# Optimization experiments

Measured on AMD Instinct MI355X. Metric: run time of the kernel, lower is better.

## Reference

```python
import jax, jax.numpy as jnp
import numpy as np
from math import sqrt

LOCAL_WINDOW = 32
STRIDE = 64


def _sparse_mask(L):
    # L_Q == L_K path of DozerAttention:
    #  - local window: diagonals at offsets 0..local_window//2 (both signs)
    #  - strided: diagonals at offsets 0, stride+1, 2*(stride+1), ... (both signs)
    i = jnp.arange(L)[:, None]
    j = jnp.arange(L)[None, :]
    d = jnp.abs(i - j)
    local = d <= (LOCAL_WINDOW // 2)
    strided = (d % (STRIDE + 1)) == 0
    return (local | strided).astype(jnp.float32)  # [L, L]


def setup_inputs() -> dict:
    key = jax.random.key(0)
    B, L, H, D = 2, 2048, 8, 64
    kq, kk, kv = jax.random.split(key, 3)
    queries = jax.random.normal(kq, (B, L, H, D), dtype=jnp.float32)
    keys = jax.random.normal(kk, (B, L, H, D), dtype=jnp.float32)
    values = jax.random.normal(kv, (B, L, H, D), dtype=jnp.float32)
    # TriangularCausalMask: True above the diagonal -> masked with -inf
    causal = jnp.triu(jnp.ones((L, L), dtype=bool), k=1)
    attn_mask = jnp.broadcast_to(causal[None, None], (B, 1, L, L))
    return {"queries": queries, "keys": keys, "values": values, "attn_mask": attn_mask}


def reference(queries, keys, values, attn_mask):
    B, L, H, D = queries.shape
    scale = 1.0 / sqrt(D)
    sm = _sparse_mask(L)  # [L, L]
    # Original fills a zero-initialized dense score tensor only at selected key
    # columns per query row; equivalent to dense QK^T elementwise-masked by sm
    # (non-selected entries stay exactly 0, NOT -inf -- faithful quirk).
    scores = jnp.einsum('blhe,bshe->bhls', queries, keys) * sm  # [B,H,L,L]
    scores = jnp.where(attn_mask, -jnp.inf, scores)
    A = jax.nn.softmax(scale * scores, axis=-1)  # dropout p=0.0 in this config
    V = jnp.einsum('bhls,bshd->blhd', A, values)  # [B,L,H,D]
    return V
```

## Files before the change

### kernel.cpp

```cpp
#include <hip/hip_runtime.h>
#include <hip/hip_bf16.h>

#define B_ 2
#define L_ 2048
#define H_ 8
#define D_ 64
#define SP_ 65
#define NC_ 128
#define NL2_ 8
#define RS_ 512

typedef __attribute__((ext_vector_type(8))) short bf16x8;
typedef __attribute__((ext_vector_type(16))) float f32x16;

static __device__ inline short f2bf(float x) {
    return __builtin_bit_cast(short, __float2bfloat16(x));
}

static __device__ inline bf16x8 ld8_bf16(const float* __restrict__ p) {
    float4 a = *(const float4*)p;
    float4 b = *(const float4*)(p + 4);
    bf16x8 r;
    r[0]=f2bf(a.x); r[1]=f2bf(a.y); r[2]=f2bf(a.z); r[3]=f2bf(a.w);
    r[4]=f2bf(b.x); r[5]=f2bf(b.y); r[6]=f2bf(b.z); r[7]=f2bf(b.w);
    return r;
}

static __device__ inline bf16x8 ones_frag() {
    bf16x8 r;
    short o = f2bf(1.f);
    #pragma unroll
    for (int t = 0; t < 8; ++t) r[t] = o;
    return r;
}

__global__ __launch_bounds__(256) void pre_strided_k(const float* __restrict__ q,
                                                     const float* __restrict__ kk,
                                                     const float* __restrict__ v,
                                                     float* __restrict__ csum1,
                                                     float* __restrict__ csum2,
                                                     float* __restrict__ pB,
                                                     float* __restrict__ zB) {
    __shared__ float Pw[4][32][36];
    int wib  = threadIdx.x >> 6;
    int lane = threadIdx.x & 63;
    int blk  = blockIdx.x;

    if (blk < 260) {
        int u  = blk * 4 + wib;
        int bh = u / SP_;
        int r  = u % SP_;
        int h = bh & 7, b = bh >> 3;
        int half = lane >> 5, ln = lane & 31;
        const size_t base = (size_t)b * L_ * RS_ + (size_t)h * D_;

        bf16x8 bv0[2], bv1[2];
        #pragma unroll
        for (int kb = 0; kb < 2; ++kb) {
            int k0 = kb * 16 + half * 8;
            #pragma unroll
            for (int jj = 0; jj < 8; ++jj) {
                int lv = r + SP_ * (k0 + jj);
                lv = lv > L_ - 1 ? L_ - 1 : lv;
                const float* vr = v + base + (size_t)lv * RS_;
                bv0[kb][jj] = f2bf(vr[ln]);
                bv1[kb][jj] = f2bf(vr[32 + ln]);
            }
        }

        int lq = r + SP_ * ln;
        int lqc = lq > L_ - 1 ? L_ - 1 : lq;
        const float* qrow = q  + base + (size_t)lqc * RS_;
        const float* krow = kk + base + (size_t)lqc * RS_;
        f32x16 acc = {};
        #pragma unroll
        for (int kb = 0; kb < 4; ++kb) {
            bf16x8 a  = ld8_bf16(qrow + kb * 16 + half * 8);
            bf16x8 bb = ld8_bf16(krow + kb * 16 + half * 8);
            acc = __builtin_amdgcn_mfma_f32_32x32x16_bf16(a, bb, acc, 0, 0, 0);
        }
        #pragma unroll
        for (int rg = 0; rg < 16; ++rg) {
            int m = (rg & 3) + 8 * (rg >> 2) + 4 * half;
            bool act = (ln < m) && (r + SP_ * m < L_);
            Pw[wib][m][ln] = act ? (__expf(0.125f * acc[rg]) - 1.f) : 0.f;
        }
        __syncthreads();

        f32x16 p0 = {}; f32x16 p1 = {}; f32x16 po = {};
        bf16x8 ones = ones_frag();
        #pragma unroll
        for (int kb = 0; kb < 2; ++kb) {
            int k0 = kb * 16 + half * 8;
            const float* pr = &Pw[wib][ln][k0];
            float4 x = *(const float4*)pr;
            float4 y = *(const float4*)(pr + 4);
            bf16x8 ap;
            ap[0]=f2bf(x.x); ap[1]=f2bf(x.y); ap[2]=f2bf(x.z); ap[3]=f2bf(x.w);
            ap[4]=f2bf(y.x); ap[5]=f2bf(y.y); ap[6]=f2bf(y.z); ap[7]=f2bf(y.w);
            p0 = __builtin_amdgcn_mfma_f32_32x32x16_bf16(ap, bv0[kb], p0, 0, 0, 0);
            p1 = __builtin_amdgcn_mfma_f32_32x32x16_bf16(ap, bv1[kb], p1, 0, 0, 0);
            po = __builtin_amdgcn_mfma_f32_32x32x16_bf16(ap, ones,    po, 0, 0, 0);
        }
        float* pBr = pB + (size_t)bh * L_ * D_;
        float* zBr = zB + (size_t)bh * L_;
        #pragma unroll
        for (int rg = 0; rg < 16; ++rg) {
            int m = (rg & 3) + 8 * (rg >> 2) + 4 * half;
            int l = r + SP_ * m;
            if (l < L_) {
                pBr[(size_t)l * D_ + ln]      = p0[rg];
                pBr[(size_t)l * D_ + 32 + ln] = p1[rg];
                if (ln == 0) zBr[l] = po[rg];
            }
        }
    } else if (blk < 772) {
        int u = (blk - 260) * 4 + wib;
        int c = u & (NC_ - 1);
        int bh = u >> 7;
        int h = bh & 7, b = bh >> 3;
        const float* vb = v + (size_t)(b * L_ + c * 16) * RS_ + h * D_ + lane;
        float s = 0.f;
        #pragma unroll
        for (int l = 0; l < 16; ++l) s += vb[l * RS_];
        csum1[(size_t)u * D_ + lane] = s;
    } else {
        int u = (blk - 772) * 4 + wib;
        int c2 = u & 7;
        int bh = u >> 3;
        int h = bh & 7, b = bh >> 3;
        const float* vb = v + (size_t)(b * L_ + c2 * 256) * RS_ + h * D_ + lane;
        float s0 = 0.f, s1 = 0.f, s2 = 0.f, s3 = 0.f;
        for (int l = 0; l < 256; l += 4) {
            s0 += vb[(l + 0) * RS_]; s1 += vb[(l + 1) * RS_];
            s2 += vb[(l + 2) * RS_]; s3 += vb[(l + 3) * RS_];
        }
        csum2[(size_t)u * D_ + lane] = (s0 + s1) + (s2 + s3);
    }
}

__global__ __launch_bounds__(256) void local_final_k(const float* __restrict__ q,
                                                     const float* __restrict__ kk,
                                                     const float* __restrict__ v,
                                                     const float* __restrict__ csum1,
                                                     const float* __restrict__ csum2,
                                                     const float* __restrict__ pB,
                                                     const float* __restrict__ zB,
                                                     float* __restrict__ out) {
    __shared__ float Pw[4][32][68];
    int wib  = threadIdx.x >> 6;
    int lane = threadIdx.x & 63;
    int half = lane >> 5, ln = lane & 31;
    int tile = blockIdx.x * 4 + wib;
    int bh = tile >> 6;
    int T  = (tile & 63) << 5;
    int h = bh & 7, b = bh >> 3;
    const size_t base = (size_t)b * L_ * RS_ + (size_t)h * D_;

    bf16x8 bv0[4], bv1[4];
    #pragma unroll
    for (int kb = 0; kb < 4; ++kb) {
        int k0 = kb * 16 + half * 8;
        #pragma unroll
        for (int jj = 0; jj < 8; ++jj) {
            int jr = T - 16 + k0 + jj;
            jr = jr < 0 ? 0 : (jr > L_ - 1 ? L_ - 1 : jr);
            const float* vr = v + base + (size_t)jr * RS_;
            bv0[kb][jj] = f2bf(vr[ln]);
            bv1[kb][jj] = f2bf(vr[32 + ln]);
        }
    }

    const float* qrow = q + base + (size_t)(T + ln) * RS_;
    bf16x8 aq[4];
    #pragma unroll
    for (int kb = 0; kb < 4; ++kb) aq[kb] = ld8_bf16(qrow + kb * 16 + half * 8);

    int j0 = T - 16 + ln; j0 = j0 < 0 ? 0 : j0;
    int j1 = T + 16 + ln; j1 = j1 > L_ - 1 ? L_ - 1 : j1;
    const float* kr0 = kk + base + (size_t)j0 * RS_;
    const float* kr1 = kk + base + (size_t)j1 * RS_;
    f32x16 acc0 = {}; f32x16 acc1 = {};
    #pragma unroll
    for (int kb = 0; kb < 4; ++kb) {
        bf16x8 b0 = ld8_bf16(kr0 + kb * 16 + half * 8);
        bf16x8 b1 = ld8_bf16(kr1 + kb * 16 + half * 8);
        acc0 = __builtin_amdgcn_mfma_f32_32x32x16_bf16(aq[kb], b0, acc0, 0, 0, 0);
        acc1 = __builtin_amdgcn_mfma_f32_32x32x16_bf16(aq[kb], b1, acc1, 0, 0, 0);
    }

    #pragma unroll
    for (int r = 0; r < 16; ++r) {
        int m = (r & 3) + 8 * (r >> 2) + 4 * half;
        bool a0 = (ln >= m) && (ln <= m + 16) && (T - 16 + ln >= 0);
        float w0 = a0 ? (__expf(0.125f * acc0[r]) - 1.f) : 0.f;
        if ((m < 16) && (ln >= 16) && (ln <= m + 16)) w0 += 1.f;
        bool a1 = (ln <= m - 16);
        float w1 = a1 ? (__expf(0.125f * acc1[r]) - 1.f) : 0.f;
        if ((m >= 16) && (ln <= m - 16)) w1 += 1.f;
        Pw[wib][m][ln]      = w0;
        Pw[wib][m][32 + ln] = w1;
    }
    __syncthreads();

    f32x16 p0 = {}; f32x16 p1 = {}; f32x16 po = {};
    bf16x8 ones = ones_frag();
    #pragma unroll
    for (int kb = 0; kb < 4; ++kb) {
        int k0 = kb * 16 + half * 8;
        const float* pr = &Pw[wib][ln][k0];
        float4 x = *(const float4*)pr;
        float4 y = *(const float4*)(pr + 4);
        bf16x8 ap;
        ap[0]=f2bf(x.x); ap[1]=f2bf(x.y); ap[2]=f2bf(x.z); ap[3]=f2bf(x.w);
        ap[4]=f2bf(y.x); ap[5]=f2bf(y.y); ap[6]=f2bf(y.z); ap[7]=f2bf(y.w);
        p0 = __builtin_amdgcn_mfma_f32_32x32x16_bf16(ap, bv0[kb], p0, 0, 0, 0);
        p1 = __builtin_amdgcn_mfma_f32_32x32x16_bf16(ap, bv1[kb], p1, 0, 0, 0);
        po = __builtin_amdgcn_mfma_f32_32x32x16_bf16(ap, ones,    po, 0, 0, 0);
    }

    int c2n = T >> 8;
    int c1a = (T >> 8) << 4, c1b = T >> 4;
    const float* cs2 = csum2 + (size_t)bh * NL2_ * D_;
    const float* cs1 = csum1 + (size_t)bh * NC_ * D_;
    float pr0 = 0.f, pr1 = 0.f;
    for (int cc = 0; cc < c2n; ++cc) {
        pr0 += cs2[cc * D_ + ln]; pr1 += cs2[cc * D_ + 32 + ln];
    }
    for (int cc = c1a; cc < c1b; ++cc) {
        pr0 += cs1[cc * D_ + ln]; pr1 += cs1[cc * D_ + 32 + ln];
    }
    float ch0 = cs1[c1b * D_ + ln], ch1 = cs1[c1b * D_ + 32 + ln];

    const float* pBr = pB + (size_t)bh * L_ * D_;
    const float* zBr = zB + (size_t)bh * L_;
    #pragma unroll
    for (int r = 0; r < 16; ++r) {
        int m = (r & 3) + 8 * (r >> 2) + 4 * half;
        int i = T + m;
        float e0 = pr0 + ((m & 16) ? ch0 : 0.f);
        float e1 = pr1 + ((m & 16) ? ch1 : 0.f);
        float zloc = po[r] - (float)((m & 15) + 1);
        float inv = 1.f / (zloc + zBr[i] + (float)(i + 1));
        out[base + (size_t)i * RS_ + ln]      = (p0[r] + e0 + pBr[(size_t)i * D_ + ln])      * inv;
        out[base + (size_t)i * RS_ + 32 + ln] = (p1[r] + e1 + pBr[(size_t)i * D_ + 32 + ln]) * inv;
    }
}

extern "C" void kernel_launch(void* const* d_in, const int* in_sizes, int n_in,
                              void* d_out, int out_size, void* d_ws, size_t ws_size,
                              hipStream_t stream) {
    const float* q = (const float*)d_in[0];
    const float* k = (const float*)d_in[1];
    const float* v = (const float*)d_in[2];
    float* out = (float*)d_out;

    float* csum1 = (float*)d_ws;
    float* csum2 = csum1 + (size_t)B_ * H_ * NC_ * D_;
    float* pB    = csum2 + (size_t)B_ * H_ * NL2_ * D_;
    float* zB    = pB    + (size_t)B_ * H_ * L_ * D_;

    pre_strided_k<<<804, 256, 0, stream>>>(q, k, v, csum1, csum2, pB, zB);
    local_final_k<<<256, 256, 0, stream>>>(q, k, v, csum1, csum2, pB, zB, out);
}
```

Baseline: 115.8 us.

## Move local-window attention into the partials kernel and add a lightweight combine kernel

The local-window QK/softmax/PV tiles now run in the first kernel alongside the strided and prefix-sum work. Their partial numerators and denominators are written to new workspace buffers pA/zA. The second kernel becomes a simple elementwise combine of local, strided and prefix contributions, with one wave handling 16 rows. The aim is to fill the GPU better in both launches and shorten the dependent tail, at the cost of an extra round trip of a B*H*L*D float buffer through global memory.

```diff
diff --git a/kernel.cpp b/kernel.cpp
--- a/kernel.cpp
+++ b/kernel.cpp
@@ -34,63 +34,77 @@
     return r;
 }
 
-__global__ __launch_bounds__(256) void pre_strided_k(const float* __restrict__ q,
-                                                     const float* __restrict__ kk,
-                                                     const float* __restrict__ v,
-                                                     float* __restrict__ csum1,
-                                                     float* __restrict__ csum2,
-                                                     float* __restrict__ pB,
-                                                     float* __restrict__ zB) {
-    __shared__ float Pw[4][32][36];
+__global__ __launch_bounds__(256) void partials_k(const float* __restrict__ q,
+                                                  const float* __restrict__ kk,
+                                                  const float* __restrict__ v,
+                                                  float* __restrict__ csum1,
+                                                  float* __restrict__ csum2,
+                                                  float* __restrict__ pA,
+                                                  float* __restrict__ zA,
+                                                  float* __restrict__ pB,
+                                                  float* __restrict__ zB) {
+    __shared__ float Pw[4][32][68];
     int wib  = threadIdx.x >> 6;
     int lane = threadIdx.x & 63;
-    int blk  = blockIdx.x;
-
-    if (blk < 260) {
-        int u  = blk * 4 + wib;
-        int bh = u / SP_;
-        int r  = u % SP_;
-        int h = bh & 7, b = bh >> 3;
-        int half = lane >> 5, ln = lane & 31;
+    int half = lane >> 5, ln = lane & 31;
+    int u = blockIdx.x * 4 + wib;
+
+    if (u < 1024) {
+        int bh = u >> 6;
+        int T  = (u & 63) << 5;
+        int h = bh & 7, b = bh >> 3;
         const size_t base = (size_t)b * L_ * RS_ + (size_t)h * D_;
 
-        bf16x8 bv0[2], bv1[2];
-        #pragma unroll
-        for (int kb = 0; kb < 2; ++kb) {
+        bf16x8 bv0[4], bv1[4];
+        #pragma unroll
+        for (int kb = 0; kb < 4; ++kb) {
             int k0 = kb * 16 + half * 8;
             #pragma unroll
             for (int jj = 0; jj < 8; ++jj) {
-                int lv = r + SP_ * (k0 + jj);
-                lv = lv > L_ - 1 ? L_ - 1 : lv;
-                const float* vr = v + base + (size_t)lv * RS_;
+                int jr = T - 16 + k0 + jj;
+                jr = jr < 0 ? 0 : (jr > L_ - 1 ? L_ - 1 : jr);
+                const float* vr = v + base + (size_t)jr * RS_;
                 bv0[kb][jj] = f2bf(vr[ln]);
                 bv1[kb][jj] = f2bf(vr[32 + ln]);
             }
         }
 
-        int lq = r + SP_ * ln;
-        int lqc = lq > L_ - 1 ? L_ - 1 : lq;
-        const float* qrow = q  + base + (size_t)lqc * RS_;
-        const float* krow = kk + base + (size_t)lqc * RS_;
-        f32x16 acc = {};
-        #pragma unroll
-        for (int kb = 0; kb < 4; ++kb) {
-            bf16x8 a  = ld8_bf16(qrow + kb * 16 + half * 8);
-            bf16x8 bb = ld8_bf16(krow + kb * 16 + half * 8);
-            acc = __builtin_amdgcn_mfma_f32_32x32x16_bf16(a, bb, acc, 0, 0, 0);
-        }
-        #pragma unroll
-        for (int rg = 0; rg < 16; ++rg) {
-            int m = (rg & 3) + 8 * (rg >> 2) + 4 * half;
-            bool act = (ln < m) && (r + SP_ * m < L_);
-            Pw[wib][m][ln] = act ? (__expf(0.125f * acc[rg]) - 1.f) : 0.f;
+        const float* qrow = q + base + (size_t)(T + ln) * RS_;
+        bf16x8 aq[4];
+        #pragma unroll
+        for (int kb = 0; kb < 4; ++kb) aq[kb] = ld8_bf16(qrow + kb * 16 + half * 8);
+
+        int j0 = T - 16 + ln; j0 = j0 < 0 ? 0 : j0;
+        int j1 = T + 16 + ln; j1 = j1 > L_ - 1 ? L_ - 1 : j1;
+        const float* kr0 = kk + base + (size_t)j0 * RS_;
+        const float* kr1 = kk + base + (size_t)j1 * RS_;
+        f32x16 acc0 = {}; f32x16 acc1 = {};
+        #pragma unroll
+        for (int kb = 0; kb < 4; ++kb) {
+            bf16x8 b0 = ld8_bf16(kr0 + kb * 16 + half * 8);
+            bf16x8 b1 = ld8_bf16(kr1 + kb * 16 + half * 8);
+            acc0 = __builtin_amdgcn_mfma_f32_32x32x16_bf16(aq[kb], b0, acc0, 0, 0, 0);
+            acc1 = __builtin_amdgcn_mfma_f32_32x32x16_bf16(aq[kb], b1, acc1, 0, 0, 0);
+        }
+
+        #pragma unroll
+        for (int r = 0; r < 16; ++r) {
+            int m = (r & 3) + 8 * (r >> 2) + 4 * half;
+            bool a0 = (ln >= m) && (ln <= m + 16) && (T - 16 + ln >= 0);
+            float w0 = a0 ? (__expf(0.125f * acc0[r]) - 1.f) : 0.f;
+            if ((m < 16) && (ln >= 16) && (ln <= m + 16)) w0 += 1.f;
+            bool a1 = (ln <= m - 16);
+            float w1 = a1 ? (__expf(0.125f * acc1[r]) - 1.f) : 0.f;
+            if ((m >= 16) && (ln <= m - 16)) w1 += 1.f;
+            Pw[wib][m][ln]      = w0;
+            Pw[wib][m][32 + ln] = w1;
         }
         __syncthreads();
 
         f32x16 p0 = {}; f32x16 p1 = {}; f32x16 po = {};
         bf16x8 ones = ones_frag();
         #pragma unroll
-        for (int kb = 0; kb < 2; ++kb) {
+        for (int kb = 0; kb < 4; ++kb) {
             int k0 = kb * 16 + half * 8;
             const float* pr = &Pw[wib][ln][k0];
             float4 x = *(const float4*)pr;
@@ -102,6 +116,72 @@
             p1 = __builtin_amdgcn_mfma_f32_32x32x16_bf16(ap, bv1[kb], p1, 0, 0, 0);
             po = __builtin_amdgcn_mfma_f32_32x32x16_bf16(ap, ones,    po, 0, 0, 0);
         }
+
+        float* pAr = pA + (size_t)bh * L_ * D_;
+        float* zAr = zA + (size_t)bh * L_;
+        #pragma unroll
+        for (int r = 0; r < 16; ++r) {
+            int m = (r & 3) + 8 * (r >> 2) + 4 * half;
+            int i = T + m;
+            pAr[(size_t)i * D_ + ln]      = p0[r];
+            pAr[(size_t)i * D_ + 32 + ln] = p1[r];
+            if (ln == 0) zAr[i] = po[r] - (float)((m & 15) + 1);
+        }
+    } else if (u < 2064) {
+        int us = u - 1024;
+        int bh = us / SP_;
+        int r  = us % SP_;
+        int h = bh & 7, b = bh >> 3;
+        const size_t base = (size_t)b * L_ * RS_ + (size_t)h * D_;
+
+        bf16x8 bv0[2], bv1[2];
+        #pragma unroll
+        for (int kb = 0; kb < 2; ++kb) {
+            int k0 = kb * 16 + half * 8;
+            #pragma unroll
+            for (int jj = 0; jj < 8; ++jj) {
+                int lv = r + SP_ * (k0 + jj);
+                lv = lv > L_ - 1 ? L_ - 1 : lv;
+                const float* vr = v + base + (size_t)lv * RS_;
+                bv0[kb][jj] = f2bf(vr[ln]);
+                bv1[kb][jj] = f2bf(vr[32 + ln]);
+            }
+        }
+
+        int lq = r + SP_ * ln;
+        int lqc = lq > L_ - 1 ? L_ - 1 : lq;
+        const float* qrow = q  + base + (size_t)lqc * RS_;
+        const float* krow = kk + base + (size_t)lqc * RS_;
+        f32x16 acc = {};
+        #pragma unroll
+        for (int kb = 0; kb < 4; ++kb) {
+            bf16x8 a  = ld8_bf16(qrow + kb * 16 + half * 8);
+            bf16x8 bb = ld8_bf16(krow + kb * 16 + half * 8);
+            acc = __builtin_amdgcn_mfma_f32_32x32x16_bf16(a, bb, acc, 0, 0, 0);
+        }
+        #pragma unroll
+        for (int rg = 0; rg < 16; ++rg) {
+            int m = (rg & 3) + 8 * (rg >> 2) + 4 * half;
+            bool act = (ln < m) && (r + SP_ * m < L_);
+            Pw[wib][m][ln] = act ? (__expf(0.125f * acc[rg]) - 1.f) : 0.f;
+        }
+        __syncthreads();
+
+        f32x16 p0 = {}; f32x16 p1 = {}; f32x16 po = {};
+        bf16x8 ones = ones_frag();
+        #pragma unroll
+        for (int kb = 0; kb < 2; ++kb) {
+            int k0 = kb * 16 + half * 8;
+            const float* pr = &Pw[wib][ln][k0];
+            float4 x = *(const float4*)pr;
+            float4 y = *(const float4*)(pr + 4);
+            bf16x8 ap;
+            ap[0]=f2bf(x.x); ap[1]=f2bf(x.y); ap[2]=f2bf(x.z); ap[3]=f2bf(x.w);
+            ap[4]=f2bf(y.x); ap[5]=f2bf(y.y); ap[6]=f2bf(y.z); ap[7]=f2bf(y.w);
+            p0 = __builtin_amdgcn_mfma_f32_32x32x16_bf16(ap, bv0[kb], p0, 0, 0, 0);
+            p1 = __builtin_amdgcn_mfma_f32_32x32x16_bf16(ap, bv1[kb], p1, 0, 0, 0);
+            po = __builtin_amdgcn_mfma_f32_32x32x16_bf16(ap, ones,    po, 0, 0, 0);
+        }
         float* pBr = pB + (size_t)bh * L_ * D_;
         float* zBr = zB + (size_t)bh * L_;
         #pragma unroll
@@ -114,20 +194,20 @@
                 if (ln == 0) zBr[l] = po[rg];
             }
         }
-    } else if (blk < 772) {
-        int u = (blk - 260) * 4 + wib;
-        int c = u & (NC_ - 1);
-        int bh = u >> 7;
+    } else if (u < 4112) {
+        int uc = u - 2064;
+        int c = uc & (NC_ - 1);
+        int bh = uc >> 7;
         int h = bh & 7, b = bh >> 3;
         const float* vb = v + (size_t)(b * L_ + c * 16) * RS_ + h * D_ + lane;
         float s = 0.f;
         #pragma unroll
         for (int l = 0; l < 16; ++l) s += vb[l * RS_];
-        csum1[(size_t)u * D_ + lane] = s;
+        csum1[(size_t)uc * D_ + lane] = s;
     } else {
-        int u = (blk - 772) * 4 + wib;
-        int c2 = u & 7;
-        int bh = u >> 3;
+        int uc = u - 4112;
+        int c2 = uc & 7;
+        int bh = uc >> 3;
         int h = bh & 7, b = bh >> 3;
         const float* vb = v + (size_t)(b * L_ + c2 * 256) * RS_ + h * D_ + lane;
         float s0 = 0.f, s1 = 0.f, s2 = 0.f, s3 = 0.f;
@@ -135,115 +215,44 @@
             s0 += vb[(l + 0) * RS_]; s1 += vb[(l + 1) * RS_];
             s2 += vb[(l + 2) * RS_]; s3 += vb[(l + 3) * RS_];
         }
-        csum2[(size_t)u * D_ + lane] = (s0 + s1) + (s2 + s3);
+        csum2[(size_t)uc * D_ + lane] = (s0 + s1) + (s2 + s3);
     }
 }
 
-__global__ __launch_bounds__(256) void local_final_k(const float* __restrict__ q,
-                                                     const float* __restrict__ kk,
-                                                     const float* __restrict__ v,
-                                                     const float* __restrict__ csum1,
-                                                     const float* __restrict__ csum2,
-                                                     const float* __restrict__ pB,
-                                                     const float* __restrict__ zB,
-                                                     float* __restrict__ out) {
-    __shared__ float Pw[4][32][68];
+__global__ __launch_bounds__(256) void combine_k(const float* __restrict__ csum1,
+                                                 const float* __restrict__ csum2,
+                                                 const float* __restrict__ pA,
+                                                 const float* __restrict__ zA,
+                                                 const float* __restrict__ pB,
+                                                 const float* __restrict__ zB,
+                                                 float* __restrict__ out) {
     int wib  = threadIdx.x >> 6;
     int lane = threadIdx.x & 63;
-    int half = lane >> 5, ln = lane & 31;
-    int tile = blockIdx.x * 4 + wib;
-    int bh = tile >> 6;
-    int T  = (tile & 63) << 5;
+    int u = blockIdx.x * 4 + wib;
+    int bh = u >> 7;
+    int g  = u & 127;
+    int i0 = g << 4;
     int h = bh & 7, b = bh >> 3;
-    const size_t base = (size_t)b * L_ * RS_ + (size_t)h * D_;
-
-    bf16x8 bv0[4], bv1[4];
-    #pragma unroll
-    for (int kb = 0; kb < 4; ++kb) {
-        int k0 = kb * 16 + half * 8;
-        #pragma unroll
-        for (int jj = 0; jj < 8; ++jj) {
-            int jr = T - 16 + k0 + jj;
-            jr = jr < 0 ? 0 : (jr > L_ - 1 ? L_ - 1 : jr);
-            const float* vr = v + base + (size_t)jr * RS_;
-            bv0[kb][jj] = f2bf(vr[ln]);
-            bv1[kb][jj] = f2bf(vr[32 + ln]);
-        }
-    }
-
-    const float* qrow = q + base + (size_t)(T + ln) * RS_;
-    bf16x8 aq[4];
-    #pragma unroll
-    for (int kb = 0; kb < 4; ++kb) aq[kb] = ld8_bf16(qrow + kb * 16 + half * 8);
-
-    int j0 = T - 16 + ln; j0 = j0 < 0 ? 0 : j0;
-    int j1 = T + 16 + ln; j1 = j1 > L_ - 1 ? L_ - 1 : j1;
-    const float* kr0 = kk + base + (size_t)j0 * RS_;
-    const float* kr1 = kk + base + (size_t)j1 * RS_;
-    f32x16 acc0 = {}; f32x16 acc1 = {};
-    #pragma unroll
-    for (int kb = 0; kb < 4; ++kb) {
-        bf16x8 b0 = ld8_bf16(kr0 + kb * 16 + half * 8);
-        bf16x8 b1 = ld8_bf16(kr1 + kb * 16 + half * 8);
-        acc0 = __builtin_amdgcn_mfma_f32_32x32x16_bf16(aq[kb], b0, acc0, 0, 0, 0);
-        acc1 = __builtin_amdgcn_mfma_f32_32x32x16_bf16(aq[kb], b1, acc1, 0, 0, 0);
-    }
+
+    int c2 = i0 >> 8;
+    const float* cs2 = csum2 + (size_t)bh * NL2_ * D_;
+    const float* cs1 = csum1 + (size_t)bh * NC_ * D_;
+    float pr = 0.f;
+    for (int cc = 0; cc < c2; ++cc)        pr += cs2[cc * D_ + lane];
+    for (int cc = c2 << 4; cc < g; ++cc)   pr += cs1[cc * D_ + lane];
+
+    const float* pAr = pA + (size_t)bh * L_ * D_;
+    const float* pBr = pB + (size_t)bh * L_ * D_;
+    const float* zAr = zA + (size_t)bh * L_;
+    const float* zBr = zB + (size_t)bh * L_;
+    const size_t obase = (size_t)b * L_ * RS_ + (size_t)h * D_;
 
     #pragma unroll
     for (int r = 0; r < 16; ++r) {
-        int m = (r & 3) + 8 * (r >> 2) + 4 * half;
-        bool a0 = (ln >= m) && (ln <= m + 16) && (T - 16 + ln >= 0);
-        float w0 = a0 ? (__expf(0.125f * acc0[r]) - 1.f) : 0.f;
-        if ((m < 16) && (ln >= 16) && (ln <= m + 16)) w0 += 1.f;
-        bool a1 = (ln <= m - 16);
-        float w1 = a1 ? (__expf(0.125f * acc1[r]) - 1.f) : 0.f;
-        if ((m >= 16) && (ln <= m - 16)) w1 += 1.f;
-        Pw[wib][m][ln]      = w0;
-        Pw[wib][m][32 + ln] = w1;
-    }
-    __syncthreads();
-
-    f32x16 p0 = {}; f32x16 p1 = {}; f32x16 po = {};
-    bf16x8 ones = ones_frag();
-    #pragma unroll
-    for (int kb = 0; kb < 4; ++kb) {
-        int k0 = kb * 16 + half * 8;
-        const float* pr = &Pw[wib][ln][k0];
-        float4 x = *(const float4*)pr;
-        float4 y = *(const float4*)(pr + 4);
-        bf16x8 ap;
-        ap[0]=f2bf(x.x); ap[1]=f2bf(x.y); ap[2]=f2bf(x.z); ap[3]=f2bf(x.w);
-        ap[4]=f2bf(y.x); ap[5]=f2bf(y.y); ap[6]=f2bf(y.z); ap[7]=f2bf(y.w);
-        p0 = __builtin_amdgcn_mfma_f32_32x32x16_bf16(ap, bv0[kb], p0, 0, 0, 0);
-        p1 = __builtin_amdgcn_mfma_f32_32x32x16_bf16(ap, bv1[kb], p1, 0, 0, 0);
-        po = __builtin_amdgcn_mfma_f32_32x32x16_bf16(ap, ones,    po, 0, 0, 0);
-    }
-
-    int c2n = T >> 8;
-    int c1a = (T >> 8) << 4, c1b = T >> 4;
-    const float* cs2 = csum2 + (size_t)bh * NL2_ * D_;
-    const float* cs1 = csum1 + (size_t)bh * NC_ * D_;
-    float pr0 = 0.f, pr1 = 0.f;
-    for (int cc = 0; cc < c2n; ++cc) {
-        pr0 += cs2[cc * D_ + ln]; pr1 += cs2[cc * D_ + 32 + ln];
-    }
-    for (int cc = c1a; cc < c1b; ++cc) {
-        pr0 += cs1[cc * D_ + ln]; pr1 += cs1[cc * D_ + 32 + ln];
-    }
-    float ch0 = cs1[c1b * D_ + ln], ch1 = cs1[c1b * D_ + 32 + ln];
-
-    const float* pBr = pB + (size_t)bh * L_ * D_;
-    const float* zBr = zB + (size_t)bh * L_;
-    #pragma unroll
-    for (int r = 0; r < 16; ++r) {
-        int m = (r & 3) + 8 * (r >> 2) + 4 * half;
-        int i = T + m;
-        float e0 = pr0 + ((m & 16) ? ch0 : 0.f);
-        float e1 = pr1 + ((m & 16) ? ch1 : 0.f);
-        float zloc = po[r] - (float)((m & 15) + 1);
-        float inv = 1.f / (zloc + zBr[i] + (float)(i + 1));
-        out[base + (size_t)i * RS_ + ln]      = (p0[r] + e0 + pBr[(size_t)i * D_ + ln])      * inv;
-        out[base + (size_t)i * RS_ + 32 + ln] = (p1[r] + e1 + pBr[(size_t)i * D_ + 32 + ln]) * inv;
+        int i = i0 + r;
+        float num = pAr[(size_t)i * D_ + lane] + pBr[(size_t)i * D_ + lane] + pr;
+        float inv = 1.f / (zAr[i] + zBr[i] + (float)(i + 1));
+        out[obase + (size_t)i * RS_ + lane] = num * inv;
     }
 }
 
@@ -257,9 +266,11 @@
 
     float* csum1 = (float*)d_ws;
     float* csum2 = csum1 + (size_t)B_ * H_ * NC_ * D_;
-    float* pB    = csum2 + (size_t)B_ * H_ * NL2_ * D_;
+    float* pA    = csum2 + (size_t)B_ * H_ * NL2_ * D_;
+    float* zA    = pA    + (size_t)B_ * H_ * L_ * D_;
+    float* pB    = zA    + (size_t)B_ * H_ * L_;
     float* zB    = pB    + (size_t)B_ * H_ * L_ * D_;
 
-    pre_strided_k<<<804, 256, 0, stream>>>(q, k, v, csum1, csum2, pB, zB);
-    local_final_k<<<256, 256, 0, stream>>>(q, k, v, csum1, csum2, pB, zB, out);
-}
+    partials_k<<<1060, 256, 0, stream>>>(q, k, v, csum1, csum2, pA, zA, pB, zB);
+    combine_k<<<512, 256, 0, stream>>>(csum1, csum2, pA, zA, pB, zB, out);
+}
```

After: 116.4 us. About the same (+0.5%).
